# Kernel optimization log

Hardware: AMD Instinct MI355X
Metric: run time of the kernel (lower is better)

Reference implementation:

```python
import jax, jax.numpy as jnp
import numpy as np

B, S, E = 32, 128, 128
NQ, NS = 100000, 512
QN, SN = 4, 10
S_MAX = 4
NEG = -1e30


def setup_inputs() -> dict:
    key = jax.random.key(0)
    ks = jax.random.split(key, 24)
    def nrm(k, shape, sc):
        return jax.random.normal(k, shape, jnp.float32) * sc
    inp = {}
    inp['question'] = jax.random.randint(ks[0], (B, S), 0, NQ, jnp.int32)
    inp['response'] = jax.random.randint(ks[1], (B, S), 0, 2, jnp.int32)
    inp['mask'] = jax.random.randint(ks[2], (B, S), 0, 2, jnp.int32)
    inp['q_neighbors'] = jax.random.randint(ks[3], (NQ, QN), 0, NS, jnp.int32)
    inp['s_neighbors'] = jax.random.randint(ks[4], (NS, SN), 0, NQ, jnp.int32)
    sidx = jax.random.randint(ks[5], (NQ, S_MAX), 0, NS, jnp.int32)
    inp['qs_table'] = jnp.zeros((NQ, NS), jnp.float32).at[jnp.arange(NQ)[:, None], sidx].set(1.0)
    inp['emb_q'] = nrm(ks[6], (NQ, E), 1.0)
    inp['emb_s'] = nrm(ks[7], (NS, E), 1.0)
    inp['emb_r'] = nrm(ks[8], (2, E), 1.0)
    s_in = 1.0 / np.sqrt(2 * E).astype(np.float32)
    s_e = 1.0 / np.sqrt(E).astype(np.float32)
    inp['W_ih'] = nrm(ks[9], (4 * E, 2 * E), s_in)
    inp['b_ih'] = nrm(ks[10], (4 * E,), s_in)
    inp['b_hh'] = nrm(ks[11], (4 * E,), s_in)
    inp['W_agg'] = nrm(ks[12], (3, E, E), s_e)
    inp['b_agg'] = nrm(ks[13], (3, E), s_e)
    inp['W_last'] = nrm(ks[14], (E, E), s_e)
    inp['b_last'] = nrm(ks[15], (E,), s_e)
    inp['W_query'] = nrm(ks[16], (E, E), s_e)
    inp['b_query'] = nrm(ks[17], (E,), s_e)
    inp['W_key'] = nrm(ks[18], (E, E), s_e)
    inp['b_key'] = nrm(ks[19], (E,), s_e)
    inp['w_W'] = nrm(ks[20], (2 * E,), s_in)
    inp['b_W'] = nrm(ks[21], (), s_in)
    return inp


def _forward(question, response, mask, q_neighbors, s_neighbors, qs_table,
             emb_q, emb_s, emb_r, W_ih, b_ih, b_hh, W_agg, b_agg, W_last, b_last,
             W_query, b_query, W_key, b_key, w_W, b_W):
    Bq, Sq = question.shape
    Ed = emb_q.shape[1]
    AGG = W_agg.shape[0]
    w_q, w_k = w_W[:Ed], w_W[Ed:]
    c_pad = jnp.tanh(b_query) @ w_k  # attention logit piece of an all-zero padded state
    pos = jnp.arange(Sq)

    def step(state_history, xs):
        t, q_t, r_t, m_t, q_next = xs
        # ---- multi-hop neighbor gather (q -> s -> q -> s) ----
        n1 = q_neighbors[q_t]              # [B,QN] skill ids
        n2 = s_neighbors[n1]               # [B,QN,SN] question ids
        n3 = q_neighbors[n2]               # [B,QN,SN,QN] skill ids
        e = [emb_q[q_t], emb_s[n1], emb_q[n2], emb_s[n3]]
        # triangular mean-aggregate (dropout is identity in eval mode)
        for i in range(AGG):
            for j in range(AGG - i):
                e[j] = jnp.tanh((e[j + 1].mean(-2) + e[j]) @ W_agg[j].T + b_agg[j])
        agg = jnp.tanh(e[0] @ W_last.T + b_last)
        emb_qt = jnp.where((m_t == 1)[:, None], agg, emb_q[q_t])
        # ---- LSTMCell with zero initial (h, c): W_hh @ 0 drops out, b_hh remains ----
        x = jnp.concatenate([emb_qt, emb_r[r_t]], -1)
        gates = x @ W_ih.T + b_ih + b_hh
        gi, gf, gg, go = jnp.split(gates, 4, -1)
        h = jax.nn.sigmoid(go) * jnp.tanh(jax.nn.sigmoid(gi) * jnp.tanh(gg))
        # ---- skills related to next question; zero-padded rows contribute exactly 0 ----
        vals, sidx = jax.lax.top_k(qs_table[q_next], S_MAX)
        emb_sk = emb_s[sidx] * (vals > 0.0)[..., None]
        qs_concat = jnp.concatenate([emb_q[q_next][:, None], emb_sk], 1)  # [B,1+S_MAX,E]
        # ---- hard recap: history steps whose question is a 2-hop neighbor of q_next ----
        q_rel = s_neighbors[q_neighbors[q_next]].reshape(Bq, -1)          # [B,QN*SN]
        matches = (question[:, :, None] == q_rel[:, None, :]).any(-1) & (pos[None, :] < t)
        n_sel = matches.sum(-1)
        P = (jnp.max(n_sel) - n_sel).astype(jnp.float32)  # zero-pad count to per-batch max
        # ---- predict: MLP_W(concat(Q,K)) is rank-1 => logit = a[b,q] + c[b,s] ----
        a = jnp.tanh(qs_concat @ W_key.T + b_key) @ w_q + b_W             # [B,Qd]
        c_hist = jnp.tanh(state_history @ W_query.T + b_query) @ w_k      # [B,S]
        c_cur = jnp.tanh(h @ W_query.T + b_query) @ w_k                   # [B]
        lh = jnp.where(matches[:, None, :], a[:, :, None] + c_hist[:, None, :], NEG)
        lc = a + c_cur[:, None]
        lp = a + c_pad
        m = jnp.maximum(jnp.maximum(lh.max(-1), lc), lp)
        Eh = jnp.exp(lh - m[:, :, None])
        Ec = jnp.exp(lc - m)
        Ep = jnp.exp(lp - m)
        g_hist = jnp.einsum('bqe,bse->bqs', qs_concat, state_history)
        g_cur = jnp.einsum('bqe,be->bq', qs_concat, h)
        denom = Eh.sum(-1) + Ec + P[:, None] * Ep  # zero-pad states counted analytically
        num = (Eh * g_hist).sum(-1) + Ec * g_cur   # pads multiply g=0 -> no numerator term
        y = jax.nn.sigmoid(jnp.sum(num / denom, axis=1))
        # original skips the state write at t == 0 (slot 0 stays zero forever)
        state_history = state_history.at[:, t].set(jnp.where(t > 0, h, jnp.zeros_like(h)))
        return state_history, y

    ts = jnp.arange(Sq - 1)
    xs = (ts, question[:, :-1].T, response[:, :-1].T, mask[:, :-1].T, question[:, 1:].T)
    init = jnp.zeros((Bq, Sq, Ed), jnp.float32)
    _, ys = jax.lax.scan(step, init, xs)
    return jnp.zeros((Bq, Sq), jnp.float32).at[:, 0].set(0.5).at[:, 1:].set(ys.T)


def reference(question, response, mask, q_neighbors, s_neighbors, qs_table,
              emb_q, emb_s, emb_r, W_ih, b_ih, b_hh, W_agg, b_agg, W_last, b_last,
              W_query, b_query, W_key, b_key, w_W, b_W):
    return _forward(question, response, mask, q_neighbors, s_neighbors, qs_table,
                    emb_q, emb_s, emb_r, W_ih, b_ih, b_hh, W_agg, b_agg, W_last, b_last,
                    W_query, b_query, W_key, b_key, w_W, b_W)
```

## Files before the change

### kernel.cpp

```cpp
#include <hip/hip_runtime.h>
#include <stdint.h>

#define NB 32
#define SEQ 128
#define EMB 128
#define NSTEP 127
#define NS 512

__device__ __forceinline__ float ftanh(float x){ float e=__expf(2.f*x); return 1.f-2.f/(e+1.f); }
__device__ __forceinline__ float fsig(float x){ return 1.f/(1.f+__expf(-x)); }
__device__ __forceinline__ float4 ld4(const float* p){ return *(const float4*)p; }

#define FMA4(acc, xv, a0, a1, a2, a3) \
  acc.x = fmaf(xv.x, a0.x, fmaf(xv.y, a1.x, fmaf(xv.z, a2.x, fmaf(xv.w, a3.x, acc.x)))); \
  acc.y = fmaf(xv.x, a0.y, fmaf(xv.y, a1.y, fmaf(xv.z, a2.y, fmaf(xv.w, a3.y, acc.y)))); \
  acc.z = fmaf(xv.x, a0.z, fmaf(xv.y, a1.z, fmaf(xv.z, a2.z, fmaf(xv.w, a3.z, acc.z)))); \
  acc.w = fmaf(xv.x, a0.w, fmaf(xv.y, a1.w, fmaf(xv.z, a2.w, fmaf(xv.w, a3.w, acc.w))));

template<int K, int XS>
__device__ __forceinline__ void gemm8(const float* __restrict__ WT, int NEtot,
                                      const float* Xl, const float* __restrict__ bias,
                                      float* outb)
{
  const int tid = threadIdx.x;
  const int et = tid & 31;
  const int rt = tid >> 5;
  const float* wp = WT + et*4;
  const float* xr = Xl + rt*XS;
  constexpr int G = K/4;
  float4 acc = {0.f,0.f,0.f,0.f};
  float4 w0 = ld4(wp);
  float4 w1 = ld4(wp + NEtot);
  float4 w2 = ld4(wp + 2*NEtot);
  float4 w3 = ld4(wp + 3*NEtot);
  const float* wq = wp + (size_t)4*NEtot;
  float4 m0 = ld4(wq);
  float4 m1 = ld4(wq + NEtot);
  float4 m2 = ld4(wq + 2*NEtot);
  float4 m3 = ld4(wq + 3*NEtot);
  #pragma unroll 2
  for (int g = 0; g + 2 < G; g += 2) {
    const float* wa = wp + (size_t)(4*(g+2))*NEtot;
    float4 n0 = ld4(wa);
    float4 n1 = ld4(wa + NEtot);
    float4 n2 = ld4(wa + 2*NEtot);
    float4 n3 = ld4(wa + 3*NEtot);
    float4 xa = ld4(xr + 4*g);
    FMA4(acc, xa, w0, w1, w2, w3);
    w0=n0; w1=n1; w2=n2; w3=n3;
    const float* wb = wp + (size_t)(4*(g+3))*NEtot;
    float4 o0 = ld4(wb);
    float4 o1 = ld4(wb + NEtot);
    float4 o2 = ld4(wb + 2*NEtot);
    float4 o3 = ld4(wb + 3*NEtot);
    float4 xb = ld4(xr + 4*(g+1));
    FMA4(acc, xb, m0, m1, m2, m3);
    m0=o0; m1=o1; m2=o2; m3=o3;
  }
  {
    float4 xa = ld4(xr + 4*(G-2));
    FMA4(acc, xa, w0, w1, w2, w3);
    float4 xb = ld4(xr + 4*(G-1));
    FMA4(acc, xb, m0, m1, m2, m3);
  }
  float4 bb = ld4(bias + et*4);
  acc.x+=bb.x; acc.y+=bb.y; acc.z+=bb.z; acc.w+=bb.w;
  *(float4*)(outb + rt*132 + et*4) = acc;
}

__global__ __launch_bounds__(256) void k_T(
    const float* __restrict__ W_agg, const float* __restrict__ W_last,
    const float* __restrict__ W_query, const float* __restrict__ W_ih,
    const float* __restrict__ b_ih, const float* __restrict__ b_hh,
    const float* __restrict__ b_query, const float* __restrict__ w_W,
    float* __restrict__ WT012, float* __restrict__ WLT, float* __restrict__ WQT,
    float* __restrict__ WIHT, float* __restrict__ BIH, float* __restrict__ CPAD,
    float* __restrict__ G1, int* __restrict__ Pmaxi)
{
  const int gid = blockIdx.x*256 + threadIdx.x;
  const int gsz = gridDim.x*256;
  for (int i = gid; i < 49152; i += gsz) {
    int j = i >> 14, rem = i & 16383, k = rem >> 7, e = rem & 127;
    WT012[i] = W_agg[j*16384 + e*128 + k];
  }
  for (int i = gid; i < 16384; i += gsz) {
    int k = i >> 7, e = i & 127;
    WLT[i] = W_last[e*128 + k];
    WQT[i] = W_query[e*128 + k];
  }
  for (int i = gid; i < 131072; i += gsz) {
    int k = i >> 9, e = i & 511;
    WIHT[i] = W_ih[e*256 + k];
  }
  for (int i = gid; i < 65536; i += gsz) G1[i] = 0.f;
  if (gid < 512) BIH[gid] = b_ih[gid] + b_hh[gid];
  if (gid < 128) Pmaxi[gid] = 0;
  if (blockIdx.x == 0) {
    __shared__ float red[256];
    float v = (threadIdx.x < 128) ? ftanh(b_query[threadIdx.x]) * w_W[128 + threadIdx.x] : 0.f;
    red[threadIdx.x] = v; __syncthreads();
    #pragma unroll
    for (int s = 128; s > 0; s >>= 1) {
      if (threadIdx.x < s) red[threadIdx.x] += red[threadIdx.x + s];
      __syncthreads();
    }
    if (threadIdx.x == 0) CPAD[0] = red[0];
  }
}

__global__ __launch_bounds__(128) void k_pre(
    const int* __restrict__ s_neighbors, const int* __restrict__ q_neighbors,
    const float* __restrict__ emb_q, const float* __restrict__ emb_s,
    const float* __restrict__ WT012, const float* __restrict__ b_agg,
    float* __restrict__ E1, float* __restrict__ G1)
{
  __shared__ float XA[4*132];
  __shared__ float XB[4*132];
  __shared__ int idx[40];
  __shared__ int n3[16];
  const int tid = threadIdx.x;
  const int blk = blockIdx.x;
  if (blk < 128) {
    const int s0 = blk*4;
    if (tid < 40) idx[tid] = s_neighbors[s0*10 + tid];
    __syncthreads();
    {
      int r = tid >> 5, e4 = (tid & 31) << 2;
      float4 a = ld4(emb_s + (size_t)(s0+r)*128 + e4);
      float sx=0,sy=0,sz=0,sw=0;
      #pragma unroll
      for (int jj = 0; jj < 10; ++jj) {
        float4 q = ld4(emb_q + (size_t)idx[r*10+jj]*128 + e4);
        sx+=q.x; sy+=q.y; sz+=q.z; sw+=q.w;
      }
      float4 o; o.x=a.x+0.1f*sx; o.y=a.y+0.1f*sy; o.z=a.z+0.1f*sz; o.w=a.w+0.1f*sw;
      *(float4*)(XA + r*132 + e4) = o;
    }
    __syncthreads();
    gemm8<128,132>(WT012 + 16384, 128, XA, b_agg + 128, XB);
    __syncthreads();
    for (int f = tid; f < 512; f += 128) {
      int r = f >> 7, e = f & 127;
      E1[(size_t)(s0+r)*128 + e] = ftanh(XB[r*132 + e]);
    }
  } else {
    const int p0 = (blk-128)*4;
    if (tid < 4) idx[tid] = s_neighbors[p0 + tid];
    __syncthreads();
    if (tid < 16) n3[tid] = q_neighbors[(size_t)idx[tid>>2]*4 + (tid&3)];
    __syncthreads();
    {
      int r = tid >> 5, e4 = (tid & 31) << 2;
      float4 a = ld4(emb_q + (size_t)idx[r]*128 + e4);
      float sx=0,sy=0,sz=0,sw=0;
      #pragma unroll
      for (int k = 0; k < 4; ++k) {
        float4 q = ld4(emb_s + (size_t)n3[r*4+k]*128 + e4);
        sx+=q.x; sy+=q.y; sz+=q.z; sw+=q.w;
      }
      float4 o; o.x=a.x+0.25f*sx; o.y=a.y+0.25f*sy; o.z=a.z+0.25f*sz; o.w=a.w+0.25f*sw;
      *(float4*)(XA + r*132 + e4) = o;
    }
    __syncthreads();
    gemm8<128,132>(WT012 + 32768, 128, XA, b_agg + 256, XB);
    __syncthreads();
    for (int f = tid; f < 512; f += 128) {
      int r = f >> 7, e = f & 127;
      atomicAdd(&G1[(size_t)((p0+r)/10)*128 + e], ftanh(XB[r*132 + e]));
    }
  }
}

__global__ __launch_bounds__(128) void k_pre2(
    const float* __restrict__ E1, const float* __restrict__ G1,
    const float* __restrict__ WT012, const float* __restrict__ b_agg,
    float* __restrict__ E2)
{
  __shared__ float XA[4*132];
  __shared__ float XB[4*132];
  const int tid = threadIdx.x;
  const int s0 = blockIdx.x*4;
  for (int f = tid; f < 512; f += 128) {
    int r = f >> 7, e = f & 127;
    XA[r*132 + e] = 0.1f*G1[(size_t)(s0+r)*128 + e] + E1[(size_t)(s0+r)*128 + e];
  }
  __syncthreads();
  gemm8<128,132>(WT012 + 16384, 128, XA, b_agg + 128, XB);
  __syncthreads();
  for (int f = tid; f < 512; f += 128) {
    int r = f >> 7, e = f & 127;
    E2[(size_t)(s0+r)*128 + e] = ftanh(XB[r*132 + e]);
  }
}

__global__ __launch_bounds__(128) void k_chain(
    const int* __restrict__ question, const int* __restrict__ response,
    const int* __restrict__ maskp, const int* __restrict__ q_neighbors,
    const float* __restrict__ emb_q, const float* __restrict__ emb_s,
    const float* __restrict__ emb_r,
    const float* __restrict__ WT012, const float* __restrict__ WLT,
    const float* __restrict__ WQT, const float* __restrict__ WIHT,
    const float* __restrict__ BIH,
    const float* __restrict__ b_agg, const float* __restrict__ b_last,
    const float* __restrict__ b_query, const float* __restrict__ w_W,
    const float* __restrict__ E1, const float* __restrict__ E2,
    float* __restrict__ Hfull, float* __restrict__ Cq)
{
  __shared__ float XA[4*132];
  __shared__ float XB[4*132];
  __shared__ float M1[4*132];
  __shared__ float M2[4*132];
  __shared__ float XC[4*264];
  __shared__ int qts[4], rts[4], mts[4], n1s[16];

  const int tid = threadIdx.x;
  const int blk = blockIdx.x;

  if (tid < 4) {
    int rid = blk*4 + tid;
    int b = rid / 127, t = rid - b*127;
    qts[tid] = question[b*SEQ + t];
    rts[tid] = response[b*SEQ + t];
    mts[tid] = maskp[b*SEQ + t];
  }
  __syncthreads();
  if (tid < 16) n1s[tid] = q_neighbors[(size_t)qts[tid>>2]*4 + (tid&3)];
  __syncthreads();
  {
    int r = tid >> 5, e4 = (tid & 31) << 2;
    const int* nn = n1s + r*4;
    float4 a = ld4(emb_q + (size_t)qts[r]*128 + e4);
    float s1x=0,s1y=0,s1z=0,s1w=0, s2x=0,s2y=0,s2z=0,s2w=0, s3x=0,s3y=0,s3z=0,s3w=0;
    #pragma unroll
    for (int i = 0; i < 4; ++i) {
      float4 q1 = ld4(emb_s + (size_t)nn[i]*128 + e4);
      float4 q2 = ld4(E1 + (size_t)nn[i]*128 + e4);
      float4 q3 = ld4(E2 + (size_t)nn[i]*128 + e4);
      s1x+=q1.x; s1y+=q1.y; s1z+=q1.z; s1w+=q1.w;
      s2x+=q2.x; s2y+=q2.y; s2z+=q2.z; s2w+=q2.w;
      s3x+=q3.x; s3y+=q3.y; s3z+=q3.z; s3w+=q3.w;
    }
    float4 o; o.x=a.x+0.25f*s1x; o.y=a.y+0.25f*s1y; o.z=a.z+0.25f*s1z; o.w=a.w+0.25f*s1w;
    *(float4*)(XA + r*132 + e4) = o;
    float4 p; p.x=0.25f*s2x; p.y=0.25f*s2y; p.z=0.25f*s2z; p.w=0.25f*s2w;
    *(float4*)(M1 + r*132 + e4) = p;
    float4 u; u.x=0.25f*s3x; u.y=0.25f*s3y; u.z=0.25f*s3z; u.w=0.25f*s3w;
    *(float4*)(M2 + r*132 + e4) = u;
  }
  __syncthreads();
  gemm8<128,132>(WT012, 128, XA, b_agg, XB);
  __syncthreads();
  for (int f = tid; f < 528; f += 128) XB[f] = M1[f] + ftanh(XB[f]);
  __syncthreads();
  gemm8<128,132>(WT012, 128, XB, b_agg, XA);
  __syncthreads();
  for (int f = tid; f < 528; f += 128) XA[f] = M2[f] + ftanh(XA[f]);
  __syncthreads();
  gemm8<128,132>(WT012, 128, XA, b_agg, XB);
  __syncthreads();
  for (int f = tid; f < 528; f += 128) XB[f] = ftanh(XB[f]);
  __syncthreads();
  gemm8<128,132>(WLT, 128, XB, b_last, XA);
  __syncthreads();
  for (int f = tid; f < 512; f += 128) {
    int r = f >> 7, e = f & 127;
    float agg = ftanh(XA[r*132 + e]);
    XC[r*264 + e] = (mts[r] == 1) ? agg : emb_q[(size_t)qts[r]*128 + e];
    XC[r*264 + 128 + e] = emb_r[rts[r]*128 + e];
  }
  __syncthreads();
  gemm8<256,264>(WIHT,       512, XC, BIH,       XA);
  gemm8<256,264>(WIHT + 256, 512, XC, BIH + 256, XB);
  gemm8<256,264>(WIHT + 384, 512, XC, BIH + 384, M1);
  __syncthreads();
  for (int f = tid; f < 512; f += 128) {
    int r = f >> 7, e = f & 127;
    float gi = XA[r*132 + e], gg = XB[r*132 + e], go = M1[r*132 + e];
    float h = fsig(go) * ftanh(fsig(gi) * ftanh(gg));
    XC[r*264 + e] = h;
    Hfull[(size_t)(blk*4 + r)*128 + e] = h;
  }
  __syncthreads();
  gemm8<128,264>(WQT, 128, XC, b_query, XA);
  __syncthreads();
  {
    const int et = tid & 31, rt = tid >> 5;
    float4 o = ld4(XA + rt*132 + et*4);
    float4 wv = ld4(w_W + 128 + et*4);
    float s = ftanh(o.x)*wv.x + ftanh(o.y)*wv.y + ftanh(o.z)*wv.z + ftanh(o.w)*wv.w;
    #pragma unroll
    for (int off = 16; off > 0; off >>= 1) s += __shfl_down(s, off);
    if (et == 0) Cq[blk*4 + rt] = s;
  }
}

__global__ __launch_bounds__(64) void k_match(
    const int* __restrict__ question, const int* __restrict__ q_neighbors,
    const int* __restrict__ s_neighbors,
    int* __restrict__ nsel, unsigned long long* __restrict__ mwords,
    int* __restrict__ Pmaxi)
{
  __shared__ int qr[40];
  const int tid = threadIdx.x;
  const int t = blockIdx.x;
  const int b = blockIdx.y;
  const int q_next = question[b*SEQ + t + 1];
  if (tid < 40)
    qr[tid] = s_neighbors[(size_t)q_neighbors[(size_t)q_next*4 + tid/10]*10 + tid%10];
  __syncthreads();
  int q0 = question[b*SEQ + tid];
  int q1 = question[b*SEQ + 64 + tid];
  bool p0 = false, p1 = false;
  #pragma unroll 8
  for (int i = 0; i < 40; ++i) { p0 |= (q0 == qr[i]); p1 |= (q1 == qr[i]); }
  p0 &= (tid < t);
  p1 &= (64 + tid < t);
  unsigned long long w0 = __ballot(p0);
  unsigned long long w1 = __ballot(p1);
  if (tid == 0) {
    mwords[((size_t)b*NSTEP + t)*2 + 0] = w0;
    mwords[((size_t)b*NSTEP + t)*2 + 1] = w1;
    int ns = __popcll(w0) + __popcll(w1);
    nsel[b*NSTEP + t] = ns;
    atomicMax(&Pmaxi[t], ns);
  }
}

__device__ __forceinline__ float wredsum(float v) {
  #pragma unroll
  for (int o = 32; o > 0; o >>= 1) v += __shfl_down(v, o);
  return v;
}
__device__ __forceinline__ float wredmax(float v) {
  #pragma unroll
  for (int o = 32; o > 0; o >>= 1) v = fmaxf(v, __shfl_down(v, o));
  return v;
}

__global__ __launch_bounds__(128) void k_attn(
    const int* __restrict__ question, const float* __restrict__ qs_table,
    const float* __restrict__ emb_q, const float* __restrict__ emb_s,
    const float* __restrict__ CPAD,
    const float* __restrict__ Hfull, const float* __restrict__ Cq,
    const int* __restrict__ nsel, const unsigned long long* __restrict__ mwords,
    const int* __restrict__ Pmaxi, float* __restrict__ out)
{
  __shared__ float us[128];
  __shared__ int cols[8];
  __shared__ int cnt;
  __shared__ float smx[2];
  __shared__ float s3[2][3];
  const int tid = threadIdx.x;
  const int wid = tid >> 6;
  const int bid = blockIdx.x;
  const int b = bid / NSTEP, t = bid % NSTEP;
  const size_t bt = (size_t)b*NSTEP + t;
  const int q_next = question[b*SEQ + t + 1];

  if (tid == 0) cnt = 0;
  __syncthreads();
  {
    float4 v = ld4(qs_table + (size_t)q_next*NS + tid*4);
    if (v.x > 0.f) { int p = atomicAdd(&cnt, 1); if (p < 8) cols[p] = tid*4; }
    if (v.y > 0.f) { int p = atomicAdd(&cnt, 1); if (p < 8) cols[p] = tid*4+1; }
    if (v.z > 0.f) { int p = atomicAdd(&cnt, 1); if (p < 8) cols[p] = tid*4+2; }
    if (v.w > 0.f) { int p = atomicAdd(&cnt, 1); if (p < 8) cols[p] = tid*4+3; }
  }
  __syncthreads();
  const int nc = min(cnt, 4);
  {
    float ue = emb_q[(size_t)q_next*EMB + tid];
    for (int i = 0; i < nc; ++i) ue += emb_s[(size_t)cols[i]*EMB + tid];
    us[tid] = ue;
  }
  const float c_pad = CPAD[0];
  const float P = (float)(Pmaxi[t] - nsel[bt]);

  const unsigned long long w0 = mwords[bt*2 + 0];
  const unsigned long long w1 = mwords[bt*2 + 1];
  const bool matched = (tid < 64) ? ((w0 >> tid) & 1ull)
                                  : ((w1 >> (tid - 64)) & 1ull);
  const float c_cur = Cq[bt];
  float Cp = matched ? ((tid == 0) ? c_pad : Cq[(size_t)b*NSTEP + tid]) : -3.0e38f;
  float mh = wredmax(Cp);
  if ((tid & 63) == 0) smx[wid] = mh;
  __syncthreads();
  float M = fmaxf(fmaxf(smx[0], smx[1]), fmaxf(c_cur, c_pad));
  float wgt = matched ? __expf(Cp - M) : 0.f;
  float dotp = 0.f;
  if (matched && tid >= 1) {
    const float* hp = Hfull + ((size_t)b*NSTEP + tid)*EMB;
    float s = 0.f;
    #pragma unroll 8
    for (int e = 0; e < 128; e += 4) {
      float4 h4 = ld4(hp + e);
      s = fmaf(us[e],h4.x, fmaf(us[e+1],h4.y, fmaf(us[e+2],h4.z, fmaf(us[e+3],h4.w, s))));
    }
    dotp = s;
  }
  float gcp = us[tid] * Hfull[bt*EMB + tid];
  float a0 = wredsum(wgt);
  float a1 = wredsum(wgt * dotp);
  float a2 = wredsum(gcp);
  if ((tid & 63) == 0) { s3[wid][0] = a0; s3[wid][1] = a1; s3[wid][2] = a2; }
  __syncthreads();
  if (tid == 0) {
    float Sexp = s3[0][0] + s3[1][0];
    float Snum = s3[0][1] + s3[1][1];
    float gc   = s3[0][2] + s3[1][2];
    float Ec = __expf(c_cur - M), Ep = __expf(c_pad - M);
    float D = Sexp + Ec + P * Ep;
    float numt = Snum + Ec * gc;
    out[b*SEQ + t + 1] = fsig(numt / D);
    if (t == 0) out[b*SEQ] = 0.5f;
  }
}

extern "C" void kernel_launch(void* const* d_in, const int* in_sizes, int n_in,
                              void* d_out, int out_size, void* d_ws, size_t ws_size,
                              hipStream_t stream) {
  const int* question    = (const int*)d_in[0];
  const int* response    = (const int*)d_in[1];
  const int* maskp       = (const int*)d_in[2];
  const int* q_neighbors = (const int*)d_in[3];
  const int* s_neighbors = (const int*)d_in[4];
  const float* qs_table  = (const float*)d_in[5];
  const float* emb_q     = (const float*)d_in[6];
  const float* emb_s     = (const float*)d_in[7];
  const float* emb_r     = (const float*)d_in[8];
  const float* W_ih      = (const float*)d_in[9];
  const float* b_ih      = (const float*)d_in[10];
  const float* b_hh      = (const float*)d_in[11];
  const float* W_agg     = (const float*)d_in[12];
  const float* b_agg     = (const float*)d_in[13];
  const float* W_last    = (const float*)d_in[14];
  const float* b_last    = (const float*)d_in[15];
  const float* W_query   = (const float*)d_in[16];
  const float* b_query   = (const float*)d_in[17];
  const float* w_W       = (const float*)d_in[20];
  float* out = (float*)d_out;

  float* ws = (float*)d_ws;
  float* WT012 = ws;
  float* WLT   = ws + 49152;
  float* WQT   = ws + 65536;
  float* WIHT  = ws + 81920;
  float* BIH   = ws + 212992;
  float* CPAD  = ws + 213504;
  float* E1    = ws + 213520;
  float* G1    = ws + 279056;
  float* E2    = ws + 344592;
  float* Hfull = ws + 410128;
  float* Cq    = ws + 930320;
  int*   Pmaxi = (int*)(ws + 934384);
  int*   nselp = (int*)(ws + 934512);
  unsigned long long* mwords =
      (unsigned long long*)(((uintptr_t)(ws + 938576) + 15) & ~(uintptr_t)15);

  k_T<<<dim3(512), dim3(256), 0, stream>>>(
      W_agg, W_last, W_query, W_ih, b_ih, b_hh, b_query, w_W,
      WT012, WLT, WQT, WIHT, BIH, CPAD, G1, Pmaxi);
  k_pre<<<dim3(1408), dim3(128), 0, stream>>>(
      s_neighbors, q_neighbors, emb_q, emb_s, WT012, b_agg, E1, G1);
  k_pre2<<<dim3(128), dim3(128), 0, stream>>>(E1, G1, WT012, b_agg, E2);
  k_chain<<<dim3(1016), dim3(128), 0, stream>>>(
      question, response, maskp, q_neighbors, emb_q, emb_s, emb_r,
      WT012, WLT, WQT, WIHT, BIH, b_agg, b_last, b_query, w_W,
      E1, E2, Hfull, Cq);
  k_match<<<dim3(NSTEP, NB), dim3(64), 0, stream>>>(
      question, q_neighbors, s_neighbors, nselp, mwords, Pmaxi);
  k_attn<<<dim3(NB*NSTEP), dim3(128), 0, stream>>>(
      question, qs_table, emb_q, emb_s, CPAD, Hfull, Cq,
      nselp, mwords, Pmaxi, out);
}
```

Measured before the change: 427.0 us.

## Fuse neighbor-match kernel into chain kernel and process 8 rows per block

The separate k_match launch is folded into k_chain, which now uses 256 threads and handles 8 (batch, step) rows per block instead of 4. The match logic broadcasts the 40 second-hop question ids with wave shuffles rather than through shared memory. This removes one kernel launch and lets each block's weight reads serve twice as many rows. The catch is that gemm8 is a template written for 128 threads and 4 rows, so running it with 256 threads and 8-row buffers may be incorrect unless that helper already generalises.

```diff
diff --git a/kernel.cpp b/kernel.cpp
--- a/kernel.cpp
+++ b/kernel.cpp
@@ -193,9 +193,10 @@
   }
 }
 
-__global__ __launch_bounds__(128) void k_chain(
+__global__ __launch_bounds__(256) void k_chain(
     const int* __restrict__ question, const int* __restrict__ response,
     const int* __restrict__ maskp, const int* __restrict__ q_neighbors,
+    const int* __restrict__ s_neighbors,
     const float* __restrict__ emb_q, const float* __restrict__ emb_s,
     const float* __restrict__ emb_r,
     const float* __restrict__ WT012, const float* __restrict__ WLT,
@@ -204,32 +205,35 @@
     const float* __restrict__ b_agg, const float* __restrict__ b_last,
     const float* __restrict__ b_query, const float* __restrict__ w_W,
     const float* __restrict__ E1, const float* __restrict__ E2,
-    float* __restrict__ Hfull, float* __restrict__ Cq)
-{
-  __shared__ float XA[4*132];
-  __shared__ float XB[4*132];
-  __shared__ float M1[4*132];
-  __shared__ float M2[4*132];
-  __shared__ float XC[4*264];
-  __shared__ int qts[4], rts[4], mts[4], n1s[16];
+    float* __restrict__ Hfull, float* __restrict__ Cq,
+    int* __restrict__ nsel, unsigned long long* __restrict__ mwords,
+    int* __restrict__ Pmaxi)
+{
+  __shared__ float XA[8*132];
+  __shared__ float XB[8*132];
+  __shared__ float M1[8*132];
+  __shared__ float M2[8*132];
+  __shared__ float XC[8*264];
+  __shared__ int qts[8], rts[8], mts[8], n1s[32];
 
   const int tid = threadIdx.x;
   const int blk = blockIdx.x;
 
-  if (tid < 4) {
-    int rid = blk*4 + tid;
+  if (tid < 8) {
+    int rid = blk*8 + tid;
     int b = rid / 127, t = rid - b*127;
     qts[tid] = question[b*SEQ + t];
     rts[tid] = response[b*SEQ + t];
     mts[tid] = maskp[b*SEQ + t];
   }
   __syncthreads();
-  if (tid < 16) n1s[tid] = q_neighbors[(size_t)qts[tid>>2]*4 + (tid&3)];
-  __syncthreads();
-  {
-    int r = tid >> 5, e4 = (tid & 31) << 2;
-    const int* nn = n1s + r*4;
-    float4 a = ld4(emb_q + (size_t)qts[r]*128 + e4);
+  if (tid < 32) n1s[tid] = q_neighbors[(size_t)qts[tid>>2]*4 + (tid&3)];
+  __syncthreads();
+  {
+    const int e4 = (tid & 31) << 2;
+    const int rr = tid >> 5;
+    const int* nn = n1s + rr*4;
+    float4 a = ld4(emb_q + (size_t)qts[rr]*128 + e4);
     float s1x=0,s1y=0,s1z=0,s1w=0, s2x=0,s2y=0,s2z=0,s2w=0, s3x=0,s3y=0,s3z=0,s3w=0;
     #pragma unroll
     for (int i = 0; i < 4; ++i) {
@@ -241,28 +245,28 @@
       s3x+=q3.x; s3y+=q3.y; s3z+=q3.z; s3w+=q3.w;
     }
     float4 o; o.x=a.x+0.25f*s1x; o.y=a.y+0.25f*s1y; o.z=a.z+0.25f*s1z; o.w=a.w+0.25f*s1w;
-    *(float4*)(XA + r*132 + e4) = o;
+    *(float4*)(XA + rr*132 + e4) = o;
     float4 p; p.x=0.25f*s2x; p.y=0.25f*s2y; p.z=0.25f*s2z; p.w=0.25f*s2w;
-    *(float4*)(M1 + r*132 + e4) = p;
+    *(float4*)(M1 + rr*132 + e4) = p;
     float4 u; u.x=0.25f*s3x; u.y=0.25f*s3y; u.z=0.25f*s3z; u.w=0.25f*s3w;
-    *(float4*)(M2 + r*132 + e4) = u;
+    *(float4*)(M2 + rr*132 + e4) = u;
   }
   __syncthreads();
   gemm8<128,132>(WT012, 128, XA, b_agg, XB);
   __syncthreads();
-  for (int f = tid; f < 528; f += 128) XB[f] = M1[f] + ftanh(XB[f]);
+  for (int f = tid; f < 1056; f += 256) XB[f] = M1[f] + ftanh(XB[f]);
   __syncthreads();
   gemm8<128,132>(WT012, 128, XB, b_agg, XA);
   __syncthreads();
-  for (int f = tid; f < 528; f += 128) XA[f] = M2[f] + ftanh(XA[f]);
+  for (int f = tid; f < 1056; f += 256) XA[f] = M2[f] + ftanh(XA[f]);
   __syncthreads();
   gemm8<128,132>(WT012, 128, XA, b_agg, XB);
   __syncthreads();
-  for (int f = tid; f < 528; f += 128) XB[f] = ftanh(XB[f]);
+  for (int f = tid; f < 1056; f += 256) XB[f] = ftanh(XB[f]);
   __syncthreads();
   gemm8<128,132>(WLT, 128, XB, b_last, XA);
   __syncthreads();
-  for (int f = tid; f < 512; f += 128) {
+  for (int f = tid; f < 1024; f += 256) {
     int r = f >> 7, e = f & 127;
     float agg = ftanh(XA[r*132 + e]);
     XC[r*264 + e] = (mts[r] == 1) ? agg : emb_q[(size_t)qts[r]*128 + e];
@@ -273,56 +277,56 @@
   gemm8<256,264>(WIHT + 256, 512, XC, BIH + 256, XB);
   gemm8<256,264>(WIHT + 384, 512, XC, BIH + 384, M1);
   __syncthreads();
-  for (int f = tid; f < 512; f += 128) {
+  for (int f = tid; f < 1024; f += 256) {
     int r = f >> 7, e = f & 127;
     float gi = XA[r*132 + e], gg = XB[r*132 + e], go = M1[r*132 + e];
     float h = fsig(go) * ftanh(fsig(gi) * ftanh(gg));
     XC[r*264 + e] = h;
-    Hfull[(size_t)(blk*4 + r)*128 + e] = h;
+    Hfull[(size_t)(blk*8 + r)*128 + e] = h;
   }
   __syncthreads();
   gemm8<128,264>(WQT, 128, XC, b_query, XA);
   __syncthreads();
   {
-    const int et = tid & 31, rt = tid >> 5;
-    float4 o = ld4(XA + rt*132 + et*4);
+    const int et = tid & 31, rr = tid >> 5;
     float4 wv = ld4(w_W + 128 + et*4);
+    float4 o = ld4(XA + rr*132 + et*4);
     float s = ftanh(o.x)*wv.x + ftanh(o.y)*wv.y + ftanh(o.z)*wv.z + ftanh(o.w)*wv.w;
     #pragma unroll
     for (int off = 16; off > 0; off >>= 1) s += __shfl_down(s, off);
-    if (et == 0) Cq[blk*4 + rt] = s;
-  }
-}
-
-__global__ __launch_bounds__(64) void k_match(
-    const int* __restrict__ question, const int* __restrict__ q_neighbors,
-    const int* __restrict__ s_neighbors,
-    int* __restrict__ nsel, unsigned long long* __restrict__ mwords,
-    int* __restrict__ Pmaxi)
-{
-  __shared__ int qr[40];
-  const int tid = threadIdx.x;
-  const int t = blockIdx.x;
-  const int b = blockIdx.y;
-  const int q_next = question[b*SEQ + t + 1];
-  if (tid < 40)
-    qr[tid] = s_neighbors[(size_t)q_neighbors[(size_t)q_next*4 + tid/10]*10 + tid%10];
-  __syncthreads();
-  int q0 = question[b*SEQ + tid];
-  int q1 = question[b*SEQ + 64 + tid];
-  bool p0 = false, p1 = false;
-  #pragma unroll 8
-  for (int i = 0; i < 40; ++i) { p0 |= (q0 == qr[i]); p1 |= (q1 == qr[i]); }
-  p0 &= (tid < t);
-  p1 &= (64 + tid < t);
-  unsigned long long w0 = __ballot(p0);
-  unsigned long long w1 = __ballot(p1);
-  if (tid == 0) {
-    mwords[((size_t)b*NSTEP + t)*2 + 0] = w0;
-    mwords[((size_t)b*NSTEP + t)*2 + 1] = w1;
-    int ns = __popcll(w0) + __popcll(w1);
-    nsel[b*NSTEP + t] = ns;
-    atomicMax(&Pmaxi[t], ns);
+    if (et == 0) Cq[blk*8 + rr] = s;
+  }
+  {
+    const int wv = tid >> 6;
+    const int ln = tid & 63;
+    for (int rr = wv; rr < 8; rr += 4) {
+      int rid = blk*8 + rr;
+      int b = rid / 127, t = rid - b*127;
+      int q_next = question[b*SEQ + t + 1];
+      int qrv = 0;
+      if (ln < 40)
+        qrv = s_neighbors[(size_t)q_neighbors[(size_t)q_next*4 + ln/10]*10 + ln%10];
+      int q0 = question[b*SEQ + ln];
+      int q1 = question[b*SEQ + 64 + ln];
+      bool p0 = false, p1 = false;
+      #pragma unroll 8
+      for (int i = 0; i < 40; ++i) {
+        int qv = __shfl(qrv, i);
+        p0 |= (q0 == qv); p1 |= (q1 == qv);
+      }
+      p0 &= (ln < t);
+      p1 &= (64 + ln < t);
+      unsigned long long w0 = __ballot(p0);
+      unsigned long long w1 = __ballot(p1);
+      if (ln == 0) {
+        size_t bt = (size_t)b*NSTEP + t;
+        mwords[bt*2 + 0] = w0;
+        mwords[bt*2 + 1] = w1;
+        int ns = __popcll(w0) + __popcll(w1);
+        nsel[bt] = ns;
+        atomicMax(&Pmaxi[t], ns);
+      }
+    }
   }
 }
 
@@ -463,12 +467,10 @@
   k_pre<<<dim3(1408), dim3(128), 0, stream>>>(
       s_neighbors, q_neighbors, emb_q, emb_s, WT012, b_agg, E1, G1);
   k_pre2<<<dim3(128), dim3(128), 0, stream>>>(E1, G1, WT012, b_agg, E2);
-  k_chain<<<dim3(1016), dim3(128), 0, stream>>>(
-      question, response, maskp, q_neighbors, emb_q, emb_s, emb_r,
+  k_chain<<<dim3(508), dim3(256), 0, stream>>>(
+      question, response, maskp, q_neighbors, s_neighbors, emb_q, emb_s, emb_r,
       WT012, WLT, WQT, WIHT, BIH, b_agg, b_last, b_query, w_W,
-      E1, E2, Hfull, Cq);
-  k_match<<<dim3(NSTEP, NB), dim3(64), 0, stream>>>(
-      question, q_neighbors, s_neighbors, nselp, mwords, Pmaxi);
+      E1, E2, Hfull, Cq, nselp, mwords, Pmaxi);
   k_attn<<<dim3(NB*NSTEP), dim3(128), 0, stream>>>(
       question, qs_table, emb_q, emb_s, CPAD, Hfull, Cq,
       nselp, mwords, Pmaxi, out);
```

New measurement: 418.6 us. -2.0%, faster.
